# Kernel optimization log

Hardware: AMD Instinct MI355X
Metric: run time of the kernel (lower is better)

## Reference

```python
import jax, jax.numpy as jnp
import numpy as np

N_PAPER = 100000
N_AUTHOR = 50000
D = 128
UNITS = 128
E = 500000


def setup_inputs() -> dict:
    key = jax.random.key(0)
    ks = jax.random.split(key, 10)
    s = 1.0 / np.sqrt(D)
    return {
        "x_paper": jax.random.normal(ks[0], (N_PAPER, D), jnp.float32),
        "x_author": jax.random.normal(ks[1], (N_AUTHOR, D), jnp.float32),
        "W_cites": jax.random.normal(ks[2], (D, UNITS), jnp.float32) * s,
        "W_writes": jax.random.normal(ks[3], (D, UNITS), jnp.float32) * s,
        "W_self": jax.random.normal(ks[4], (D, UNITS), jnp.float32) * s,
        "bias": jnp.zeros((UNITS,), jnp.float32),
        "cites_src": jax.random.randint(ks[5], (E,), 0, N_PAPER, jnp.int32),
        "cites_dst": jax.random.randint(ks[6], (E,), 0, N_PAPER, jnp.int32),
        "writes_src": jax.random.randint(ks[7], (E,), 0, N_AUTHOR, jnp.int32),
        "writes_dst": jax.random.randint(ks[8], (E,), 0, N_PAPER, jnp.int32),
    }


def reference(x_paper, x_author, W_cites, W_writes, W_self, bias,
              cites_src, cites_dst, writes_src, writes_dst) -> jnp.ndarray:
    n_recv = x_paper.shape[0]

    # Per-edge-set: transform sender node states, gather to edges, segment-sum to receivers.
    def pool(x_sender, W, src, dst):
        h = x_sender @ W                                  # [n_sender, units]
        msgs = jnp.take(h, src, axis=0)                   # [E, units] broadcast to edges
        pooled = jax.ops.segment_sum(msgs, dst, num_segments=n_recv)
        deg = jax.ops.segment_sum(jnp.ones_like(dst, jnp.float32), dst,
                                  num_segments=n_recv)
        return pooled, deg

    pooled_c, deg_c = pool(x_paper, W_cites, cites_src, cites_dst)
    pooled_w, deg_w = pool(x_author, W_writes, writes_src, writes_dst)

    # Self-loop transform counts as one more "in-edge" per node for mean.
    self_vals = x_paper @ W_self                          # [n_recv, units]
    summed = pooled_c + pooled_w + self_vals
    total_deg = deg_c + deg_w + 1.0                       # [n_recv]

    # tf.math.divide_no_nan semantics
    mean = jnp.where(total_deg[:, None] != 0.0, summed / total_deg[:, None], 0.0)
    return jax.nn.relu(mean + bias)
```

## Files before the change

### kernel.cpp

```cpp
#include <hip/hip_runtime.h>
#include <hip/hip_bf16.h>

#define NP     100000
#define NA     50000
#define DIM    128
#define UNITS  128
#define NEDGE  500000
#define NE2    (2 * NEDGE)

#define GEMM_ROWS 32
#define GP (NP / GEMM_ROWS)
#define GA ((NA + GEMM_ROWS - 1) / GEMM_ROWS)

#define CHUNK  1024
#define NCHUNK ((NP + CHUNK - 1) / CHUNK)

__global__ __launch_bounds__(256, 2) void gemm_all(
    const float* __restrict__ x_paper, const float* __restrict__ x_author,
    const float* __restrict__ W_cites, const float* __restrict__ W_writes,
    const float* __restrict__ W_self,
    float* __restrict__ H, float* __restrict__ out)
{
    const float* X; const float* W; float* Ho; int nrows; int bb;
    if (blockIdx.x < GP) {
        X = x_paper;  W = W_cites;  Ho = H;                      nrows = NP; bb = blockIdx.x;
    } else if (blockIdx.x < GP + GA) {
        X = x_author; W = W_writes; Ho = H + (size_t)NP * UNITS; nrows = NA; bb = blockIdx.x - GP;
    } else {
        X = x_paper;  W = W_self;   Ho = out;                    nrows = NP; bb = blockIdx.x - GP - GA;
    }

    __shared__ float Wl[DIM * UNITS];
    __shared__ float Xl[GEMM_ROWS * DIM];

    const int tid  = threadIdx.x;
    const int row0 = bb * GEMM_ROWS;

    const float4* W4  = (const float4*)W;
    float4*       Wl4 = (float4*)Wl;
#pragma unroll
    for (int i = 0; i < 16; ++i)
        Wl4[i * 256 + tid] = W4[i * 256 + tid];

    const float4* X4  = (const float4*)(X + (size_t)row0 * DIM);
    float4*       Xl4 = (float4*)Xl;
#pragma unroll
    for (int i = 0; i < 4; ++i) {
        int idx = i * 256 + tid;
        if (row0 + (idx >> 5) < nrows)
            Xl4[idx] = X4[idx];
    }
    __syncthreads();

    const int ug = tid & 31;
    const int rg = tid >> 5;
    const int r0 = rg * 4;

    float acc[4][4];
#pragma unroll
    for (int r = 0; r < 4; ++r)
#pragma unroll
        for (int j = 0; j < 4; ++j) acc[r][j] = 0.0f;

#pragma unroll 4
    for (int kk = 0; kk < 32; ++kk) {
        float4 xv[4], wv[4];
#pragma unroll
        for (int r = 0; r < 4; ++r) xv[r] = Xl4[(r0 + r) * 32 + kk];
#pragma unroll
        for (int i = 0; i < 4; ++i) wv[i] = Wl4[(kk * 4 + i) * 32 + ug];
#pragma unroll
        for (int r = 0; r < 4; ++r) {
            const float xr0 = xv[r].x, xr1 = xv[r].y, xr2 = xv[r].z, xr3 = xv[r].w;
            acc[r][0] = fmaf(xr0, wv[0].x, acc[r][0]);
            acc[r][1] = fmaf(xr0, wv[0].y, acc[r][1]);
            acc[r][2] = fmaf(xr0, wv[0].z, acc[r][2]);
            acc[r][3] = fmaf(xr0, wv[0].w, acc[r][3]);
            acc[r][0] = fmaf(xr1, wv[1].x, acc[r][0]);
            acc[r][1] = fmaf(xr1, wv[1].y, acc[r][1]);
            acc[r][2] = fmaf(xr1, wv[1].z, acc[r][2]);
            acc[r][3] = fmaf(xr1, wv[1].w, acc[r][3]);
            acc[r][0] = fmaf(xr2, wv[2].x, acc[r][0]);
            acc[r][1] = fmaf(xr2, wv[2].y, acc[r][1]);
            acc[r][2] = fmaf(xr2, wv[2].z, acc[r][2]);
            acc[r][3] = fmaf(xr2, wv[2].w, acc[r][3]);
            acc[r][0] = fmaf(xr3, wv[3].x, acc[r][0]);
            acc[r][1] = fmaf(xr3, wv[3].y, acc[r][1]);
            acc[r][2] = fmaf(xr3, wv[3].z, acc[r][2]);
            acc[r][3] = fmaf(xr3, wv[3].w, acc[r][3]);
        }
    }

    float4* H4 = (float4*)Ho;
#pragma unroll
    for (int r = 0; r < 4; ++r) {
        int row = row0 + r0 + r;
        if (row < nrows) {
            float4 v; v.x = acc[r][0]; v.y = acc[r][1]; v.z = acc[r][2]; v.w = acc[r][3];
            H4[(size_t)row * 32 + ug] = v;
        }
    }
}

__global__ __launch_bounds__(256) void zero_count(int* __restrict__ count)
{
    int i = blockIdx.x * 256 + threadIdx.x;
    if (i < NP) count[i] = 0;
}

__global__ __launch_bounds__(256) void hist_k(
    const int* __restrict__ c_dst, const int* __restrict__ w_dst,
    int* __restrict__ count)
{
    int i = blockIdx.x * 256 + threadIdx.x;
    if (i >= NE2) return;
    int d = (i < NEDGE) ? c_dst[i] : w_dst[i - NEDGE];
    atomicAdd(&count[d], 1);
}

__global__ __launch_bounds__(256) void scanA(
    const int* __restrict__ count, int* __restrict__ csum)
{
    __shared__ int red[256];
    const int c = blockIdx.x, t = threadIdx.x;
    const int base = c * CHUNK + t * 4;
    int s = 0;
#pragma unroll
    for (int r = 0; r < 4; ++r)
        if (base + r < NP) s += count[base + r];
    red[t] = s; __syncthreads();
#pragma unroll
    for (int off = 128; off > 0; off >>= 1) {
        if (t < off) red[t] += red[t + off];
        __syncthreads();
    }
    if (t == 0) csum[c] = red[0];
}

__global__ __launch_bounds__(128) void scanB(
    const int* __restrict__ csum, int* __restrict__ coff)
{
    __shared__ int ts[128];
    const int t = threadIdx.x;
    const int v = (t < NCHUNK) ? csum[t] : 0;
    ts[t] = v; __syncthreads();
    for (int off = 1; off < 128; off <<= 1) {
        int x = (t >= off) ? ts[t - off] : 0;
        __syncthreads();
        ts[t] += x;
        __syncthreads();
    }
    if (t < NCHUNK) coff[t] = ts[t] - v;
}

__global__ __launch_bounds__(256) void scanC(
    const int* __restrict__ count, const int* __restrict__ coff,
    int* __restrict__ cursor)
{
    __shared__ int ts[256];
    const int c = blockIdx.x, t = threadIdx.x;
    const int base = c * CHUNK + t * 4;
    int v0 = 0, v1 = 0, v2 = 0, v3 = 0;
    if (base + 0 < NP) v0 = count[base + 0];
    if (base + 1 < NP) v1 = count[base + 1];
    if (base + 2 < NP) v2 = count[base + 2];
    if (base + 3 < NP) v3 = count[base + 3];
    const int s = v0 + v1 + v2 + v3;
    ts[t] = s; __syncthreads();
    for (int off = 1; off < 256; off <<= 1) {
        int x = (t >= off) ? ts[t - off] : 0;
        __syncthreads();
        ts[t] += x;
        __syncthreads();
    }
    int excl = ts[t] - s + coff[c];
    if (base + 0 < NP) cursor[base + 0] = excl;
    if (base + 1 < NP) cursor[base + 1] = excl + v0;
    if (base + 2 < NP) cursor[base + 2] = excl + v0 + v1;
    if (base + 3 < NP) cursor[base + 3] = excl + v0 + v1 + v2;
}

__global__ __launch_bounds__(256) void fill_k(
    const int* __restrict__ c_src, const int* __restrict__ c_dst,
    const int* __restrict__ w_src, const int* __restrict__ w_dst,
    int* __restrict__ cursor, int* __restrict__ eidx)
{
    int i = blockIdx.x * 256 + threadIdx.x;
    if (i >= NE2) return;
    int d, val;
    if (i < NEDGE) { d = c_dst[i];         val = c_src[i]; }
    else           { int j = i - NEDGE; d = w_dst[j]; val = NP + w_src[j]; }
    int pos = atomicAdd(&cursor[d], 1);
    eidx[pos] = val;
}

__global__ __launch_bounds__(256) void gather_fused(
    const float* __restrict__ H, const int* __restrict__ eidx,
    const int* __restrict__ cursor, const float* __restrict__ bias,
    float* __restrict__ out)
{
    const int tid = threadIdx.x;
    const int g = tid >> 5, l = tid & 31;
    const int n = blockIdx.x * 8 + g;

    float4 acc = ((const float4*)out)[(size_t)n * 32 + l];

    const int start = (n == 0) ? 0 : cursor[n - 1];
    const int end   = cursor[n];
    const float4* H4 = (const float4*)H;
    int e_next = (start < end) ? eidx[start] : 0;
    for (int j = start; j < end; ++j) {
        const int e = e_next;
        if (j + 1 < end) e_next = eidx[j + 1];
        const float4 v = H4[(size_t)e * 32 + l];
        acc.x += v.x; acc.y += v.y; acc.z += v.z; acc.w += v.w;
    }

    const float inv = 1.0f / (float)(end - start + 1);
    const float4 b = ((const float4*)bias)[l];
    float4 o;
    o.x = fmaxf(fmaf(acc.x, inv, b.x), 0.0f);
    o.y = fmaxf(fmaf(acc.y, inv, b.y), 0.0f);
    o.z = fmaxf(fmaf(acc.z, inv, b.z), 0.0f);
    o.w = fmaxf(fmaf(acc.w, inv, b.w), 0.0f);
    ((float4*)out)[(size_t)n * 32 + l] = o;
}

extern "C" void kernel_launch(void* const* d_in, const int* in_sizes, int n_in,
                              void* d_out, int out_size, void* d_ws, size_t ws_size,
                              hipStream_t stream)
{
    const float* x_paper    = (const float*)d_in[0];
    const float* x_author   = (const float*)d_in[1];
    const float* W_cites    = (const float*)d_in[2];
    const float* W_writes   = (const float*)d_in[3];
    const float* W_self     = (const float*)d_in[4];
    const float* bias       = (const float*)d_in[5];
    const int*   cites_src  = (const int*)d_in[6];
    const int*   cites_dst  = (const int*)d_in[7];
    const int*   writes_src = (const int*)d_in[8];
    const int*   writes_dst = (const int*)d_in[9];
    float* out = (float*)d_out;

    char* ws = (char*)d_ws;
    float* H      = (float*)(ws);
    int*   eidx   = (int*)(ws + 76800000);
    int*   count  = (int*)(ws + 80800000);
    int*   cursor = (int*)(ws + 81200000);
    int*   csum   = (int*)(ws + 81600000);
    int*   coff   = (int*)(ws + 81600512);

    gemm_all<<<2 * GP + GA, 256, 0, stream>>>(
        x_paper, x_author, W_cites, W_writes, W_self, H, out);

    zero_count<<<(NP + 255) / 256, 256, 0, stream>>>(count);
    hist_k<<<(NE2 + 255) / 256, 256, 0, stream>>>(cites_dst, writes_dst, count);
    scanA<<<NCHUNK, 256, 0, stream>>>(count, csum);
    scanB<<<1, 128, 0, stream>>>(csum, coff);
    scanC<<<NCHUNK, 256, 0, stream>>>(count, coff, cursor);
    fill_k<<<(NE2 + 255) / 256, 256, 0, stream>>>(
        cites_src, cites_dst, writes_src, writes_dst, cursor, eidx);

    gather_fused<<<NP / 8, 256, 0, stream>>>(H, eidx, cursor, bias, out);
}
```

Baseline: 434.5 us.

## Replace FP32 SIMT GEMM with split-bf16 MFMA GEMM (hi/lo, three products)

Moves the three dense transforms from scalar FP32 FMAs onto MFMA bf16 instructions. Each fp32 operand is split into a high and a low bf16 part, and three MFMA products (hi*hi, hi*lo, lo*hi) approximate fp32 accuracy. The tile grows to 128 rows with an XOR-swizzled shared layout to avoid bank conflicts. In exchange it pays for conversion work on every tile load, including re-splitting W in every block, uses 128KB of LDS with one block per CU, and loses a little precision.

```diff
diff --git a/kernel.cpp b/kernel.cpp
--- a/kernel.cpp
+++ b/kernel.cpp
@@ -8,96 +8,152 @@
 #define NEDGE  500000
 #define NE2    (2 * NEDGE)
 
-#define GEMM_ROWS 32
-#define GP (NP / GEMM_ROWS)
-#define GA ((NA + GEMM_ROWS - 1) / GEMM_ROWS)
+#define BM   128
+#define GPB  ((NP + BM - 1) / BM)
+#define GAB  ((NA + BM - 1) / BM)
 
 #define CHUNK  1024
 #define NCHUNK ((NP + CHUNK - 1) / CHUNK)
 
-__global__ __launch_bounds__(256, 2) void gemm_all(
+typedef __attribute__((ext_vector_type(8))) short bfrag;
+typedef __attribute__((ext_vector_type(4))) float f32x4;
+
+__device__ __forceinline__ unsigned int bf_rne(float x) {
+    unsigned int u = __builtin_bit_cast(unsigned int, x);
+    u += 0x7FFFu + ((u >> 16) & 1u);
+    return u >> 16;
+}
+__device__ __forceinline__ float bf_to_f(unsigned int b) {
+    unsigned int u = b << 16;
+    return __builtin_bit_cast(float, u);
+}
+
+__global__ __launch_bounds__(256, 1) void mfma_gemm_all(
     const float* __restrict__ x_paper, const float* __restrict__ x_author,
     const float* __restrict__ W_cites, const float* __restrict__ W_writes,
     const float* __restrict__ W_self,
     float* __restrict__ H, float* __restrict__ out)
 {
     const float* X; const float* W; float* Ho; int nrows; int bb;
-    if (blockIdx.x < GP) {
+    if (blockIdx.x < GPB) {
         X = x_paper;  W = W_cites;  Ho = H;                      nrows = NP; bb = blockIdx.x;
-    } else if (blockIdx.x < GP + GA) {
-        X = x_author; W = W_writes; Ho = H + (size_t)NP * UNITS; nrows = NA; bb = blockIdx.x - GP;
+    } else if (blockIdx.x < GPB + GAB) {
+        X = x_author; W = W_writes; Ho = H + (size_t)NP * UNITS; nrows = NA; bb = blockIdx.x - GPB;
     } else {
-        X = x_paper;  W = W_self;   Ho = out;                    nrows = NP; bb = blockIdx.x - GP - GA;
-    }
-
-    __shared__ float Wl[DIM * UNITS];
-    __shared__ float Xl[GEMM_ROWS * DIM];
+        X = x_paper;  W = W_self;   Ho = out;                    nrows = NP; bb = blockIdx.x - GPB - GAB;
+    }
+
+    __shared__ unsigned short Xhi[BM * DIM];
+    __shared__ unsigned short Xlo[BM * DIM];
+    __shared__ unsigned short Whi[DIM * UNITS];
+    __shared__ unsigned short Wlo[DIM * UNITS];
 
     const int tid  = threadIdx.x;
-    const int row0 = bb * GEMM_ROWS;
-
-    const float4* W4  = (const float4*)W;
-    float4*       Wl4 = (float4*)Wl;
-#pragma unroll
-    for (int i = 0; i < 16; ++i)
-        Wl4[i * 256 + tid] = W4[i * 256 + tid];
-
-    const float4* X4  = (const float4*)(X + (size_t)row0 * DIM);
-    float4*       Xl4 = (float4*)Xl;
-#pragma unroll
-    for (int i = 0; i < 4; ++i) {
-        int idx = i * 256 + tid;
-        if (row0 + (idx >> 5) < nrows)
-            Xl4[idx] = X4[idx];
+    const int row0 = bb * BM;
+
+#pragma unroll
+    for (int i = 0; i < 8; ++i) {
+        const int item = i * 256 + tid;
+        const int n    = item & 127;
+        const int koct = item >> 7;
+        unsigned int h[8], l[8];
+#pragma unroll
+        for (int j = 0; j < 8; ++j) {
+            const float e = W[(size_t)(koct * 8 + j) * UNITS + n];
+            h[j] = bf_rne(e);
+            l[j] = bf_rne(e - bf_to_f(h[j]));
+        }
+        uint4 hv, lv;
+        hv.x = h[0] | (h[1] << 16); hv.y = h[2] | (h[3] << 16);
+        hv.z = h[4] | (h[5] << 16); hv.w = h[6] | (h[7] << 16);
+        lv.x = l[0] | (l[1] << 16); lv.y = l[2] | (l[3] << 16);
+        lv.z = l[4] | (l[5] << 16); lv.w = l[6] | (l[7] << 16);
+        const int slot = koct * 128 + n;
+        ((uint4*)Whi)[slot] = hv;
+        ((uint4*)Wlo)[slot] = lv;
+    }
+
+    const float4* X4 = (const float4*)(X + (size_t)row0 * DIM);
+#pragma unroll
+    for (int i = 0; i < 8; ++i) {
+        const int item = i * 256 + tid;
+        const int koct = item & 15;
+        const int row  = item >> 4;
+        if (row0 + row < nrows) {
+            const float4 v0 = X4[row * 32 + koct * 2];
+            const float4 v1 = X4[row * 32 + koct * 2 + 1];
+            const float e[8] = {v0.x, v0.y, v0.z, v0.w, v1.x, v1.y, v1.z, v1.w};
+            unsigned int h[8], l[8];
+#pragma unroll
+            for (int j = 0; j < 8; ++j) {
+                h[j] = bf_rne(e[j]);
+                l[j] = bf_rne(e[j] - bf_to_f(h[j]));
+            }
+            uint4 hv, lv;
+            hv.x = h[0] | (h[1] << 16); hv.y = h[2] | (h[3] << 16);
+            hv.z = h[4] | (h[5] << 16); hv.w = h[6] | (h[7] << 16);
+            lv.x = l[0] | (l[1] << 16); lv.y = l[2] | (l[3] << 16);
+            lv.z = l[4] | (l[5] << 16); lv.w = l[6] | (l[7] << 16);
+            const int slot = koct * 128 + (row ^ koct);
+            ((uint4*)Xhi)[slot] = hv;
+            ((uint4*)Xlo)[slot] = lv;
+        }
     }
     __syncthreads();
 
-    const int ug = tid & 31;
-    const int rg = tid >> 5;
-    const int r0 = rg * 4;
-
-    float acc[4][4];
-#pragma unroll
-    for (int r = 0; r < 4; ++r)
-#pragma unroll
-        for (int j = 0; j < 4; ++j) acc[r][j] = 0.0f;
-
-#pragma unroll 4
-    for (int kk = 0; kk < 32; ++kk) {
-        float4 xv[4], wv[4];
-#pragma unroll
-        for (int r = 0; r < 4; ++r) xv[r] = Xl4[(r0 + r) * 32 + kk];
-#pragma unroll
-        for (int i = 0; i < 4; ++i) wv[i] = Wl4[(kk * 4 + i) * 32 + ug];
+    const int lane = tid & 63;
+    const int wv   = tid >> 6;
+    const int wr   = (wv >> 1) * 64;
+    const int wc   = (wv & 1) * 64;
+    const int l16  = lane & 15;
+    const int q    = lane >> 4;
+
+    f32x4 acc[4][4];
+#pragma unroll
+    for (int rt = 0; rt < 4; ++rt)
+#pragma unroll
+        for (int ct = 0; ct < 4; ++ct) acc[rt][ct] = (f32x4)(0.0f);
+
+#pragma unroll
+    for (int kk = 0; kk < 4; ++kk) {
+        const int fb = kk * 4 + q;
+        bfrag ah[4], al[4], bh[4], bl[4];
+#pragma unroll
+        for (int rt = 0; rt < 4; ++rt) {
+            const int row = wr + rt * 16 + l16;
+            const int off = (fb * 128 + (row ^ fb)) * 8;
+            ah[rt] = *(const bfrag*)&Xhi[off];
+            al[rt] = *(const bfrag*)&Xlo[off];
+        }
+#pragma unroll
+        for (int ct = 0; ct < 4; ++ct) {
+            const int off = (fb * 128 + wc + ct * 16 + l16) * 8;
+            bh[ct] = *(const bfrag*)&Whi[off];
+            bl[ct] = *(const bfrag*)&Wlo[off];
+        }
+#pragma unroll
+        for (int rt = 0; rt < 4; ++rt)
+#pragma unroll
+            for (int ct = 0; ct < 4; ++ct) {
+                acc[rt][ct] = __builtin_amdgcn_mfma_f32_16x16x32_bf16(
+                    ah[rt], bh[ct], acc[rt][ct], 0, 0, 0);
+                acc[rt][ct] = __builtin_amdgcn_mfma_f32_16x16x32_bf16(
+                    ah[rt], bl[ct], acc[rt][ct], 0, 0, 0);
+                acc[rt][ct] = __builtin_amdgcn_mfma_f32_16x16x32_bf16(
+                    al[rt], bh[ct], acc[rt][ct], 0, 0, 0);
+            }
+    }
+
+#pragma unroll
+    for (int rt = 0; rt < 4; ++rt) {
 #pragma unroll
         for (int r = 0; r < 4; ++r) {
-            const float xr0 = xv[r].x, xr1 = xv[r].y, xr2 = xv[r].z, xr3 = xv[r].w;
-            acc[r][0] = fmaf(xr0, wv[0].x, acc[r][0]);
-            acc[r][1] = fmaf(xr0, wv[0].y, acc[r][1]);
-            acc[r][2] = fmaf(xr0, wv[0].z, acc[r][2]);
-            acc[r][3] = fmaf(xr0, wv[0].w, acc[r][3]);
-            acc[r][0] = fmaf(xr1, wv[1].x, acc[r][0]);
-            acc[r][1] = fmaf(xr1, wv[1].y, acc[r][1]);
-            acc[r][2] = fmaf(xr1, wv[1].z, acc[r][2]);
-            acc[r][3] = fmaf(xr1, wv[1].w, acc[r][3]);
-            acc[r][0] = fmaf(xr2, wv[2].x, acc[r][0]);
-            acc[r][1] = fmaf(xr2, wv[2].y, acc[r][1]);
-            acc[r][2] = fmaf(xr2, wv[2].z, acc[r][2]);
-            acc[r][3] = fmaf(xr2, wv[2].w, acc[r][3]);
-            acc[r][0] = fmaf(xr3, wv[3].x, acc[r][0]);
-            acc[r][1] = fmaf(xr3, wv[3].y, acc[r][1]);
-            acc[r][2] = fmaf(xr3, wv[3].z, acc[r][2]);
-            acc[r][3] = fmaf(xr3, wv[3].w, acc[r][3]);
-        }
-    }
-
-    float4* H4 = (float4*)Ho;
-#pragma unroll
-    for (int r = 0; r < 4; ++r) {
-        int row = row0 + r0 + r;
-        if (row < nrows) {
-            float4 v; v.x = acc[r][0]; v.y = acc[r][1]; v.z = acc[r][2]; v.w = acc[r][3];
-            H4[(size_t)row * 32 + ug] = v;
+            const int row = wr + rt * 16 + q * 4 + r;
+            if (row0 + row < nrows) {
+                float* dst = Ho + (size_t)(row0 + row) * UNITS + wc + l16;
+#pragma unroll
+                for (int ct = 0; ct < 4; ++ct) dst[ct * 16] = acc[rt][ct][r];
+            }
         }
     }
 }
@@ -250,7 +306,7 @@
     int*   csum   = (int*)(ws + 81600000);
     int*   coff   = (int*)(ws + 81600512);
 
-    gemm_all<<<2 * GP + GA, 256, 0, stream>>>(
+    mfma_gemm_all<<<2 * GPB + GAB, 256, 0, stream>>>(
         x_paper, x_author, W_cites, W_writes, W_self, H, out);
 
     zero_count<<<(NP + 255) / 256, 256, 0, stream>>>(count);
```

Measured after the change: 393.9 us. 1.1x faster.
